# Kernel optimization log

Hardware: AMD Instinct MI355X
Metric: run time of the kernel (lower is better)

## Reference

```python
import jax, jax.numpy as jnp
import numpy as np

V = 32000      # vocab_size
CTX = 1024     # context_length
D = 768        # n_embd
H = 12         # n_heads
HD = D // H    # head_dim
L = 6          # n_layers
DFF = 4 * D
B, S = 2, 1024
EPS = 1e-5


def _layernorm(x, w, b):
    mu = jnp.mean(x, axis=-1, keepdims=True)
    var = jnp.mean(jnp.square(x - mu), axis=-1, keepdims=True)
    return (x - mu) * jax.lax.rsqrt(var + EPS) * w + b


def setup_inputs() -> dict:
    key = jax.random.key(0)
    ks = iter(jax.random.split(key, 32))
    s = 0.02
    idx = jax.random.randint(next(ks), (B, S), 0, V)
    p = {
        "idx": idx,
        "tok_emb": jax.random.normal(next(ks), (V, D), jnp.float32) * s,
        "pos_emb": jax.random.normal(next(ks), (CTX, D), jnp.float32) * s,
        "ln1_w": jnp.ones((L, D)), "ln1_b": jnp.zeros((L, D)),
        "Wq": jax.random.normal(next(ks), (L, D, D), jnp.float32) * s,
        "bq": jnp.zeros((L, D)),
        "Wk": jax.random.normal(next(ks), (L, D, D), jnp.float32) * s,
        "bk": jnp.zeros((L, D)),
        "Wv": jax.random.normal(next(ks), (L, D, D), jnp.float32) * s,
        "bv": jnp.zeros((L, D)),
        "Wo": jax.random.normal(next(ks), (L, D, D), jnp.float32) * s,
        "bo": jnp.zeros((L, D)),
        "ln2_w": jnp.ones((L, D)), "ln2_b": jnp.zeros((L, D)),
        "W1": jax.random.normal(next(ks), (L, D, DFF), jnp.float32) * s,
        "b1": jnp.zeros((L, DFF)),
        "W2": jax.random.normal(next(ks), (L, DFF, D), jnp.float32) * s,
        "b2": jnp.zeros((L, D)),
        "lnf_w": jnp.ones((D,)), "lnf_b": jnp.zeros((D,)),
        "lm_head_w": jax.random.normal(next(ks), (D, V), jnp.float32) * s,
    }
    return p


def _forward(idx, tok_emb, pos_emb, ln1_w, ln1_b, Wq, bq, Wk, bk, Wv, bv,
             Wo, bo, ln2_w, ln2_b, W1, b1, W2, b2, lnf_w, lnf_b, lm_head_w):
    b, s = idx.shape
    x = tok_emb[idx] + pos_emb[:s]  # [B,S,D]
    mask = jnp.tril(jnp.ones((s, s), dtype=bool))  # causal
    scale = 1.0 / np.sqrt(HD)
    for l in range(L):
        # --- attention ---
        h = _layernorm(x, ln1_w[l], ln1_b[l])
        q = (h @ Wq[l] + bq[l]).reshape(b, s, H, HD).transpose(0, 2, 1, 3)
        k = (h @ Wk[l] + bk[l]).reshape(b, s, H, HD).transpose(0, 2, 1, 3)
        v = (h @ Wv[l] + bv[l]).reshape(b, s, H, HD).transpose(0, 2, 1, 3)
        att = jnp.einsum('bhqd,bhkd->bhqk', q, k) * scale
        att = jnp.where(mask, att, -jnp.inf)
        att = jax.nn.softmax(att, axis=-1)
        y = jnp.einsum('bhqk,bhkd->bhqd', att, v)
        y = y.transpose(0, 2, 1, 3).reshape(b, s, D)
        x = x + y @ Wo[l] + bo[l]
        # --- MLP ---
        h2 = _layernorm(x, ln2_w[l], ln2_b[l])
        x = x + jax.nn.relu(h2 @ W1[l] + b1[l]) @ W2[l] + b2[l]
    logits = _layernorm(x, lnf_w, lnf_b) @ lm_head_w  # [B,S,V]
    return logits


def reference(idx, tok_emb, pos_emb, ln1_w, ln1_b, Wq, bq, Wk, bk, Wv, bv,
              Wo, bo, ln2_w, ln2_b, W1, b1, W2, b2, lnf_w, lnf_b, lm_head_w):
    return _forward(idx, tok_emb, pos_emb, ln1_w, ln1_b, Wq, bq, Wk, bk, Wv,
                    bv, Wo, bo, ln2_w, ln2_b, W1, b1, W2, b2, lnf_w, lnf_b,
                    lm_head_w)
```

## Files before the change

### kernel.cpp

```cpp
#include <hip/hip_runtime.h>
#include <hip/hip_bf16.h>
#include <math.h>

#define D 768
#define NH 12
#define HD 64
#define NL 6
#define DFF 3072
#define BB 2
#define SS 1024
#define NROWS (BB*SS)
#define VOCAB 32000
#define QKVN (3*D)
#define LN_EPS 1e-5f

typedef __attribute__((ext_vector_type(8))) short bf16x8;
typedef __attribute__((ext_vector_type(4))) float f32x4;

typedef __attribute__((address_space(1))) const unsigned char* gas_ptr;
typedef __attribute__((address_space(3))) unsigned char* las_ptr;

__device__ __forceinline__ void load_lds16(const void* g, void* l) {
    __builtin_amdgcn_global_load_lds((gas_ptr)g, (las_ptr)l, 16, 0, 0);
}

__device__ __forceinline__ void storeOut(float* p, float v) { *p = v; }
__device__ __forceinline__ void storeOut(__hip_bfloat16* p, float v) { *p = __float2bfloat16(v); }
__device__ __forceinline__ ushort f2bs(float f) {
    __hip_bfloat16 h = __float2bfloat16(f);
    return *(ushort*)&h;
}

__global__ void embed_kernel(const int* __restrict__ idx, const float* __restrict__ tok,
                             const float* __restrict__ pos, float* __restrict__ x) {
    int row = blockIdx.x;
    int s = row % SS;
    int t = idx[row];
    for (int c = threadIdx.x; c < D; c += blockDim.x)
        x[row*D + c] = tok[(size_t)t*D + c] + pos[s*D + c];
}

template<typename OT>
__global__ __launch_bounds__(256) void layernorm_kernel(const float* __restrict__ x,
                                                        const float* __restrict__ w,
                                                        const float* __restrict__ b,
                                                        OT* __restrict__ out) {
    int row = blockIdx.x;
    __shared__ float l1[4], l2[4];
    int base = row * D;
    float vals[3];
    float s1 = 0.f, s2 = 0.f;
#pragma unroll
    for (int i = 0; i < 3; i++) {
        float v = x[base + threadIdx.x + i*256];
        vals[i] = v; s1 += v; s2 += v*v;
    }
#pragma unroll
    for (int o = 32; o > 0; o >>= 1) {
        s1 += __shfl_down(s1, o, 64);
        s2 += __shfl_down(s2, o, 64);
    }
    if ((threadIdx.x & 63) == 0) { l1[threadIdx.x >> 6] = s1; l2[threadIdx.x >> 6] = s2; }
    __syncthreads();
    float sum   = l1[0] + l1[1] + l1[2] + l1[3];
    float sumsq = l2[0] + l2[1] + l2[2] + l2[3];
    float mu  = sum * (1.f / D);
    float var = sumsq * (1.f / D) - mu * mu;
    float inv = rsqrtf(var + LN_EPS);
#pragma unroll
    for (int i = 0; i < 3; i++) {
        int c = threadIdx.x + i*256;
        storeOut(&out[base + c], (vals[i] - mu) * inv * w[c] + b[c]);
    }
}

__global__ __launch_bounds__(256) void transpose_cvt(const float* __restrict__ src,
                                                     __hip_bfloat16* __restrict__ dst,
                                                     int K, int N,
                                                     size_t srcLayerStride, size_t dstLayerStride,
                                                     int dstRowOff) {
    int l = blockIdx.z;
    src += (size_t)l * srcLayerStride;
    dst += (size_t)l * dstLayerStride + (size_t)dstRowOff * K;
    __shared__ float t[32][33];
    int k0 = blockIdx.x*32, n0 = blockIdx.y*32;
    int tx = threadIdx.x & 31, ty = threadIdx.x >> 5;
    for (int i = ty; i < 32; i += 8) t[i][tx] = src[(size_t)(k0+i)*N + n0+tx];
    __syncthreads();
    for (int i = ty; i < 32; i += 8) dst[(size_t)(n0+i)*K + k0+tx] = __float2bfloat16(t[tx][i]);
}

__global__ void pack_qkv_bias(const float* __restrict__ bq, const float* __restrict__ bk,
                              const float* __restrict__ bv, float* __restrict__ dst) {
    int l = blockIdx.y;
    int i = blockIdx.x*256 + threadIdx.x;
    dst[l*QKVN + i]         = bq[l*D + i];
    dst[l*QKVN + D + i]     = bk[l*D + i];
    dst[l*QKVN + 2*D + i]   = bv[l*D + i];
}

template<int BM, int BN, int CMAJ, typename OT, int RELU, int RESID, int HASB>
__global__ __launch_bounds__(256) void gemm_mfma(const ushort* __restrict__ A,
                                                 const ushort* __restrict__ BT,
                                                 const float* __restrict__ bias,
                                                 const float* __restrict__ X,
                                                 OT* __restrict__ C,
                                                 int N, int K, int gx, int gy) {
    constexpr int WTM = BM/2, WTN = BN/2;
    constexpr int FRM = BM/32, FRN = BN/32;
    __shared__ ushort As[BM][32];
    __shared__ ushort Bs[BN][32];

    int id = blockIdx.x;
    int swz = (id & 7) * (gridDim.x >> 3) + (id >> 3);
    int bx, by;
    if (CMAJ) { bx = swz / gy; by = swz - bx * gy; }
    else      { by = swz / gx; bx = swz - by * gx; }
    int bm = by * BM, bn = bx * BN;

    int tid = threadIdx.x;
    int lane = tid & 63, wid = tid >> 6;
    int wr = wid >> 1, wc = wid & 1;
    int lrow = lane >> 2;
    int lcol = (lane & 3) * 8;
    int fr = lane & 15, fc = lane >> 4;

    f32x4 acc[FRM][FRN];
#pragma unroll
    for (int i = 0; i < FRM; i++)
#pragma unroll
        for (int j = 0; j < FRN; j++)
#pragma unroll
            for (int r = 0; r < 4; r++) acc[i][j][r] = 0.f;

    for (int k0 = 0; k0 < K; k0 += 32) {
#pragma unroll
        for (int i = 0; i < BM/64; i++) {
            int rt = wid*(BM/4) + i*16;
            load_lds16(A + (size_t)(bm + rt + lrow)*K + k0 + lcol, &As[rt][0]);
        }
#pragma unroll
        for (int i = 0; i < BN/64; i++) {
            int rt = wid*(BN/4) + i*16;
            load_lds16(BT + (size_t)(bn + rt + lrow)*K + k0 + lcol, &Bs[rt][0]);
        }
        asm volatile("s_waitcnt vmcnt(0)" ::: "memory");
        __syncthreads();
        bf16x8 af[FRM], bf[FRN];
#pragma unroll
        for (int mi = 0; mi < FRM; mi++) af[mi] = *(const bf16x8*)&As[wr*WTM + mi*16 + fr][fc*8];
#pragma unroll
        for (int ni = 0; ni < FRN; ni++) bf[ni] = *(const bf16x8*)&Bs[wc*WTN + ni*16 + fr][fc*8];
#pragma unroll
        for (int mi = 0; mi < FRM; mi++)
#pragma unroll
            for (int ni = 0; ni < FRN; ni++)
                acc[mi][ni] = __builtin_amdgcn_mfma_f32_16x16x32_bf16(af[mi], bf[ni], acc[mi][ni], 0, 0, 0);
        __syncthreads();
    }
#pragma unroll
    for (int mi = 0; mi < FRM; mi++) {
#pragma unroll
        for (int r = 0; r < 4; r++) {
            int row = bm + wr*WTM + mi*16 + fc*4 + r;
#pragma unroll
            for (int ni = 0; ni < FRN; ni++) {
                int col = bn + wc*WTN + ni*16 + fr;
                float v = acc[mi][ni][r];
                if (HASB) v += bias[col];
                if (RESID) v += X[(size_t)row * N + col];
                if (RELU) v = fmaxf(v, 0.f);
                storeOut(&C[(size_t)row * N + col], v);
            }
        }
    }
}

__global__ __launch_bounds__(256) void attn_mfma(const float* __restrict__ qkv,
                                                 __hip_bfloat16* __restrict__ y) {
    const int bx = blockIdx.x;
    const int qt = 15 - (bx & 15);
    const int h  = (bx >> 4) % NH;
    const int b  = bx / (16*NH);
    const int tid  = threadIdx.x;
    const int lane = tid & 63, w = tid >> 6;
    const int fr = lane & 15, fc = lane >> 4;

    __shared__ ushort Qs[64][72];
    __shared__ ushort Ks[64][72];
    __shared__ ushort Vs[64][72];
    __shared__ ushort Ps[4][16][72];

    const int q0 = qt * 64;
    const int srow = tid >> 2, sfs = tid & 3;

    {
        const float* src = qkv + (size_t)(b*SS + q0 + srow)*QKVN + h*HD;
#pragma unroll
        for (int it = 0; it < 4; it++) {
            int d0 = sfs*4 + it*16;
            float4 v4 = *(const float4*)(src + d0);
            ushort4 u;
            u.x = f2bs(v4.x); u.y = f2bs(v4.y); u.z = f2bs(v4.z); u.w = f2bs(v4.w);
            *(ushort4*)&Qs[srow][d0] = u;
        }
    }
    bf16x8 qf[2];
#pragma unroll
    for (int s = 0; s < 2; s++) qf[s] = *(const bf16x8*)&Qs[w*16 + fr][s*32 + fc*8];

    f32x4 oacc[4];
#pragma unroll
    for (int ni = 0; ni < 4; ni++)
#pragma unroll
        for (int r = 0; r < 4; r++) oacc[ni][r] = 0.f;
    float m[4] = {-INFINITY, -INFINITY, -INFINITY, -INFINITY};
    float l[4] = {0.f, 0.f, 0.f, 0.f};

    for (int kt = 0; kt <= qt; kt++) {
        const int kv0 = kt * 64;
        __syncthreads();
        {
            const float* ksrc = qkv + (size_t)(b*SS + kv0 + srow)*QKVN + D   + h*HD;
            const float* vsrc = qkv + (size_t)(b*SS + kv0 + srow)*QKVN + 2*D + h*HD;
#pragma unroll
            for (int it = 0; it < 4; it++) {
                int d0 = sfs*4 + it*16;
                float4 kv4 = *(const float4*)(ksrc + d0);
                ushort4 u;
                u.x = f2bs(kv4.x); u.y = f2bs(kv4.y); u.z = f2bs(kv4.z); u.w = f2bs(kv4.w);
                *(ushort4*)&Ks[srow][d0] = u;
                float4 vv4 = *(const float4*)(vsrc + d0);
                Vs[d0+0][srow] = f2bs(vv4.x);
                Vs[d0+1][srow] = f2bs(vv4.y);
                Vs[d0+2][srow] = f2bs(vv4.z);
                Vs[d0+3][srow] = f2bs(vv4.w);
            }
        }
        __syncthreads();
        f32x4 sacc[4];
#pragma unroll
        for (int ni = 0; ni < 4; ni++)
#pragma unroll
            for (int r = 0; r < 4; r++) sacc[ni][r] = 0.f;
#pragma unroll
        for (int ni = 0; ni < 4; ni++)
#pragma unroll
            for (int s = 0; s < 2; s++) {
                bf16x8 kf = *(const bf16x8*)&Ks[ni*16 + fr][s*32 + fc*8];
                sacc[ni] = __builtin_amdgcn_mfma_f32_16x16x32_bf16(qf[s], kf, sacc[ni], 0, 0, 0);
            }
        if (kt == qt) {
#pragma unroll
            for (int ni = 0; ni < 4; ni++)
#pragma unroll
                for (int r = 0; r < 4; r++) {
                    float v = sacc[ni][r] * 0.125f;
                    sacc[ni][r] = (ni*16 + fr > w*16 + fc*4 + r) ? -INFINITY : v;
                }
        } else {
#pragma unroll
            for (int ni = 0; ni < 4; ni++)
#pragma unroll
                for (int r = 0; r < 4; r++) sacc[ni][r] *= 0.125f;
        }
        float p[4][4];
#pragma unroll
        for (int r = 0; r < 4; r++) {
            float mx = fmaxf(fmaxf(sacc[0][r], sacc[1][r]), fmaxf(sacc[2][r], sacc[3][r]));
#pragma unroll
            for (int o = 1; o < 16; o <<= 1) mx = fmaxf(mx, __shfl_xor(mx, o, 64));
            float mn = fmaxf(m[r], mx);
            float fac = __expf(m[r] - mn);
            float rs = 0.f;
#pragma unroll
            for (int ni = 0; ni < 4; ni++) {
                float pv = __expf(sacc[ni][r] - mn);
                p[ni][r] = pv;
                rs += pv;
            }
#pragma unroll
            for (int o = 1; o < 16; o <<= 1) rs += __shfl_xor(rs, o, 64);
            l[r] = l[r] * fac + rs;
            m[r] = mn;
#pragma unroll
            for (int ni = 0; ni < 4; ni++) oacc[ni][r] *= fac;
        }
#pragma unroll
        for (int ni = 0; ni < 4; ni++)
#pragma unroll
            for (int r = 0; r < 4; r++)
                Ps[w][fc*4 + r][ni*16 + fr] = f2bs(p[ni][r]);
        bf16x8 pa[2];
#pragma unroll
        for (int s = 0; s < 2; s++) pa[s] = *(const bf16x8*)&Ps[w][fr][s*32 + fc*8];
#pragma unroll
        for (int ni = 0; ni < 4; ni++)
#pragma unroll
            for (int s = 0; s < 2; s++) {
                bf16x8 vf = *(const bf16x8*)&Vs[ni*16 + fr][s*32 + fc*8];
                oacc[ni] = __builtin_amdgcn_mfma_f32_16x16x32_bf16(pa[s], vf, oacc[ni], 0, 0, 0);
            }
    }
#pragma unroll
    for (int r = 0; r < 4; r++) {
        float rinv = 1.f / l[r];
        int row = b*SS + q0 + w*16 + fc*4 + r;
#pragma unroll
        for (int ni = 0; ni < 4; ni++)
            y[(size_t)row*D + h*HD + ni*16 + fr] = __float2bfloat16(oacc[ni][r] * rinv);
    }
}

extern "C" void kernel_launch(void* const* d_in, const int* in_sizes, int n_in,
                              void* d_out, int out_size, void* d_ws, size_t ws_size,
                              hipStream_t stream) {
    const int*   idx  = (const int*)d_in[0];
    const float* tok  = (const float*)d_in[1];
    const float* pos  = (const float*)d_in[2];
    const float* ln1w = (const float*)d_in[3];
    const float* ln1b = (const float*)d_in[4];
    const float* Wq   = (const float*)d_in[5];
    const float* bq   = (const float*)d_in[6];
    const float* Wk   = (const float*)d_in[7];
    const float* bk   = (const float*)d_in[8];
    const float* Wv   = (const float*)d_in[9];
    const float* bv   = (const float*)d_in[10];
    const float* Wo   = (const float*)d_in[11];
    const float* bo   = (const float*)d_in[12];
    const float* ln2w = (const float*)d_in[13];
    const float* ln2b = (const float*)d_in[14];
    const float* W1   = (const float*)d_in[15];
    const float* b1   = (const float*)d_in[16];
    const float* W2   = (const float*)d_in[17];
    const float* b2   = (const float*)d_in[18];
    const float* lnfw = (const float*)d_in[19];
    const float* lnfb = (const float*)d_in[20];
    const float* lmw  = (const float*)d_in[21];
    float* out = (float*)d_out;

    char* p = (char*)d_ws;
    __hip_bfloat16* qkvT = (__hip_bfloat16*)p; p += (size_t)NL*QKVN*D*2;
    __hip_bfloat16* WoT  = (__hip_bfloat16*)p; p += (size_t)NL*D*D*2;
    __hip_bfloat16* W1T  = (__hip_bfloat16*)p; p += (size_t)NL*DFF*D*2;
    __hip_bfloat16* W2T  = (__hip_bfloat16*)p; p += (size_t)NL*D*DFF*2;
    __hip_bfloat16* lmT  = (__hip_bfloat16*)p; p += (size_t)VOCAB*D*2;
    float*          bqkv = (float*)p;          p += (size_t)NL*QKVN*4;
    float*          x    = (float*)p;          p += (size_t)NROWS*D*4;
    __hip_bfloat16* h    = (__hip_bfloat16*)p; p += (size_t)NROWS*D*2;
    float*          qkv  = (float*)p;          p += (size_t)NROWS*QKVN*4;
    __hip_bfloat16* yb   = (__hip_bfloat16*)p; p += (size_t)NROWS*D*2;
    __hip_bfloat16* a1   = (__hip_bfloat16*)p; p += (size_t)NROWS*DFF*2;

    dim3 tDD(D/32, D/32, NL);
    transpose_cvt<<<tDD, 256, 0, stream>>>(Wq, qkvT, D, D, (size_t)D*D, (size_t)QKVN*D, 0);
    transpose_cvt<<<tDD, 256, 0, stream>>>(Wk, qkvT, D, D, (size_t)D*D, (size_t)QKVN*D, D);
    transpose_cvt<<<tDD, 256, 0, stream>>>(Wv, qkvT, D, D, (size_t)D*D, (size_t)QKVN*D, 2*D);
    transpose_cvt<<<tDD, 256, 0, stream>>>(Wo, WoT, D, D, (size_t)D*D, (size_t)D*D, 0);
    transpose_cvt<<<dim3(D/32, DFF/32, NL), 256, 0, stream>>>(W1, W1T, D, DFF, (size_t)D*DFF, (size_t)DFF*D, 0);
    transpose_cvt<<<dim3(DFF/32, D/32, NL), 256, 0, stream>>>(W2, W2T, DFF, D, (size_t)DFF*D, (size_t)D*DFF, 0);
    transpose_cvt<<<dim3(D/32, VOCAB/32, 1), 256, 0, stream>>>(lmw, lmT, D, VOCAB, 0, 0, 0);
    pack_qkv_bias<<<dim3(3, NL), 256, 0, stream>>>(bq, bk, bv, bqkv);

    embed_kernel<<<NROWS, 256, 0, stream>>>(idx, tok, pos, x);

    for (int l = 0; l < NL; l++) {
        layernorm_kernel<<<NROWS, 256, 0, stream>>>(x, ln1w + l*D, ln1b + l*D, h);
        gemm_mfma<128,64,0,float,0,0,1><<<576, 256, 0, stream>>>(
            (const ushort*)h, (const ushort*)(qkvT + (size_t)l*QKVN*D),
            bqkv + (size_t)l*QKVN, nullptr, qkv, QKVN, D, QKVN/64, NROWS/128);
        attn_mfma<<<BB*NH*(SS/64), 256, 0, stream>>>(qkv, yb);
        gemm_mfma<64,64,0,float,0,1,1><<<384, 256, 0, stream>>>(
            (const ushort*)yb, (const ushort*)(WoT + (size_t)l*D*D),
            bo + (size_t)l*D, x, x, D, D, D/64, NROWS/64);
        layernorm_kernel<<<NROWS, 256, 0, stream>>>(x, ln2w + l*D, ln2b + l*D, h);
        gemm_mfma<128,128,0,__hip_bfloat16,1,0,1><<<384, 256, 0, stream>>>(
            (const ushort*)h, (const ushort*)(W1T + (size_t)l*DFF*D),
            b1 + (size_t)l*DFF, nullptr, a1, DFF, D, DFF/128, NROWS/128);
        gemm_mfma<64,64,0,float,0,1,1><<<384, 256, 0, stream>>>(
            (const ushort*)a1, (const ushort*)(W2T + (size_t)l*D*DFF),
            b2 + (size_t)l*D, x, x, D, DFF, D/64, NROWS/64);
    }
    layernorm_kernel<<<NROWS, 256, 0, stream>>>(x, lnfw, lnfb, h);
    gemm_mfma<128,128,1,float,0,0,0><<<4000, 256, 0, stream>>>(
        (const ushort*)h, (const ushort*)lmT, nullptr, nullptr, out, VOCAB, D,
        VOCAB/128, NROWS/128);
}
```

Baseline: 1.408 ms.

## Store QKV in bf16, pre-transpose V, and XOR-swizzle LDS tiles

The QKV projection now writes bf16 instead of fp32, which halves that buffer's traffic. A new kernel transposes V into a per-head [HD][S] layout so attention can fill its K/V/Q tiles with direct global-to-LDS loads instead of scalar convert-and-scatter code. LDS tiles in both the GEMM and the attention kernel use an XOR chunk swizzle to avoid bank conflicts, and the attention tiles drop their padding. The cost is an extra kernel launch per layer and more bf16 rounding on Q/K/V.

New measurement: 1.277 ms. -9.3%, faster.

```diff
diff --git a/kernel.cpp b/kernel.cpp
--- a/kernel.cpp
+++ b/kernel.cpp
@@ -90,6 +90,22 @@
     for (int i = ty; i < 32; i += 8) dst[(size_t)(n0+i)*K + k0+tx] = __float2bfloat16(t[tx][i]);
 }
 
+__global__ __launch_bounds__(256) void vtrans_kernel(const ushort* __restrict__ qkv,
+                                                     ushort* __restrict__ vt) {
+    int bh = blockIdx.z;
+    int st = blockIdx.y;
+    int dt = blockIdx.x;
+    __shared__ ushort t[32][33];
+    int tx = threadIdx.x & 31, ty = threadIdx.x >> 5;
+    int b = bh / NH, h = bh % NH;
+    int s0 = st*32, d0 = dt*32;
+    for (int i = ty; i < 32; i += 8)
+        t[i][tx] = qkv[(size_t)(b*SS + s0+i)*QKVN + 2*D + h*HD + d0 + tx];
+    __syncthreads();
+    for (int i = ty; i < 32; i += 8)
+        vt[((size_t)bh*HD + d0+i)*SS + s0 + tx] = t[tx][i];
+}
+
 __global__ void pack_qkv_bias(const float* __restrict__ bq, const float* __restrict__ bk,
                               const float* __restrict__ bv, float* __restrict__ dst) {
     int l = blockIdx.y;
@@ -122,7 +138,7 @@
     int lane = tid & 63, wid = tid >> 6;
     int wr = wid >> 1, wc = wid & 1;
     int lrow = lane >> 2;
-    int lcol = (lane & 3) * 8;
+    int lcol = (((lane & 3) ^ (lrow & 3)) * 8);
     int fr = lane & 15, fc = lane >> 4;
 
     f32x4 acc[FRM][FRN];
@@ -148,9 +164,11 @@
         __syncthreads();
         bf16x8 af[FRM], bf[FRN];
 #pragma unroll
-        for (int mi = 0; mi < FRM; mi++) af[mi] = *(const bf16x8*)&As[wr*WTM + mi*16 + fr][fc*8];
-#pragma unroll
-        for (int ni = 0; ni < FRN; ni++) bf[ni] = *(const bf16x8*)&Bs[wc*WTN + ni*16 + fr][fc*8];
+        for (int mi = 0; mi < FRM; mi++)
+            af[mi] = *(const bf16x8*)&As[wr*WTM + mi*16 + fr][(fc ^ (fr & 3))*8];
+#pragma unroll
+        for (int ni = 0; ni < FRN; ni++)
+            bf[ni] = *(const bf16x8*)&Bs[wc*WTN + ni*16 + fr][(fc ^ (fr & 3))*8];
 #pragma unroll
         for (int mi = 0; mi < FRM; mi++)
 #pragma unroll
@@ -176,7 +194,8 @@
     }
 }
 
-__global__ __launch_bounds__(256) void attn_mfma(const float* __restrict__ qkv,
+__global__ __launch_bounds__(256) void attn_mfma(const ushort* __restrict__ qkv,
+                                                 const ushort* __restrict__ vt,
                                                  __hip_bfloat16* __restrict__ y) {
     const int bx = blockIdx.x;
     const int qt = 15 - (bx & 15);
@@ -186,28 +205,25 @@
     const int lane = tid & 63, w = tid >> 6;
     const int fr = lane & 15, fc = lane >> 4;
 
-    __shared__ ushort Qs[64][72];
-    __shared__ ushort Ks[64][72];
-    __shared__ ushort Vs[64][72];
+    __shared__ ushort Qs[64][64];
+    __shared__ ushort Ks[64][64];
+    __shared__ ushort Vs[64][64];
     __shared__ ushort Ps[4][16][72];
 
     const int q0 = qt * 64;
-    const int srow = tid >> 2, sfs = tid & 3;
-
-    {
-        const float* src = qkv + (size_t)(b*SS + q0 + srow)*QKVN + h*HD;
-#pragma unroll
-        for (int it = 0; it < 4; it++) {
-            int d0 = sfs*4 + it*16;
-            float4 v4 = *(const float4*)(src + d0);
-            ushort4 u;
-            u.x = f2bs(v4.x); u.y = f2bs(v4.y); u.z = f2bs(v4.z); u.w = f2bs(v4.w);
-            *(ushort4*)&Qs[srow][d0] = u;
-        }
-    }
+    const int srow8  = lane >> 3;
+    const int schunk = (lane & 7) ^ srow8;
+
+#pragma unroll
+    for (int j = 0; j < 2; j++) {
+        int r = w*16 + j*8 + srow8;
+        load_lds16(qkv + (size_t)(b*SS + q0 + r)*QKVN + h*HD + schunk*8, &Qs[w*16 + j*8][0]);
+    }
+    asm volatile("s_waitcnt vmcnt(0)" ::: "memory");
     bf16x8 qf[2];
 #pragma unroll
-    for (int s = 0; s < 2; s++) qf[s] = *(const bf16x8*)&Qs[w*16 + fr][s*32 + fc*8];
+    for (int s = 0; s < 2; s++)
+        qf[s] = *(const bf16x8*)&Qs[w*16 + fr][((s*4 + fc) ^ (fr & 7))*8];
 
     f32x4 oacc[4];
 #pragma unroll
@@ -220,23 +236,13 @@
     for (int kt = 0; kt <= qt; kt++) {
         const int kv0 = kt * 64;
         __syncthreads();
-        {
-            const float* ksrc = qkv + (size_t)(b*SS + kv0 + srow)*QKVN + D   + h*HD;
-            const float* vsrc = qkv + (size_t)(b*SS + kv0 + srow)*QKVN + 2*D + h*HD;
-#pragma unroll
-            for (int it = 0; it < 4; it++) {
-                int d0 = sfs*4 + it*16;
-                float4 kv4 = *(const float4*)(ksrc + d0);
-                ushort4 u;
-                u.x = f2bs(kv4.x); u.y = f2bs(kv4.y); u.z = f2bs(kv4.z); u.w = f2bs(kv4.w);
-                *(ushort4*)&Ks[srow][d0] = u;
-                float4 vv4 = *(const float4*)(vsrc + d0);
-                Vs[d0+0][srow] = f2bs(vv4.x);
-                Vs[d0+1][srow] = f2bs(vv4.y);
-                Vs[d0+2][srow] = f2bs(vv4.z);
-                Vs[d0+3][srow] = f2bs(vv4.w);
-            }
-        }
+#pragma unroll
+        for (int j = 0; j < 2; j++) {
+            int r = w*16 + j*8 + srow8;
+            load_lds16(qkv + (size_t)(b*SS + kv0 + r)*QKVN + D + h*HD + schunk*8, &Ks[w*16 + j*8][0]);
+            load_lds16(vt + ((size_t)(b*NH + h)*HD + r)*SS + kv0 + schunk*8, &Vs[w*16 + j*8][0]);
+        }
+        asm volatile("s_waitcnt vmcnt(0)" ::: "memory");
         __syncthreads();
         f32x4 sacc[4];
 #pragma unroll
@@ -247,7 +253,7 @@
         for (int ni = 0; ni < 4; ni++)
 #pragma unroll
             for (int s = 0; s < 2; s++) {
-                bf16x8 kf = *(const bf16x8*)&Ks[ni*16 + fr][s*32 + fc*8];
+                bf16x8 kf = *(const bf16x8*)&Ks[ni*16 + fr][((s*4 + fc) ^ (fr & 7))*8];
                 sacc[ni] = __builtin_amdgcn_mfma_f32_16x16x32_bf16(qf[s], kf, sacc[ni], 0, 0, 0);
             }
         if (kt == qt) {
@@ -298,7 +304,7 @@
         for (int ni = 0; ni < 4; ni++)
 #pragma unroll
             for (int s = 0; s < 2; s++) {
-                bf16x8 vf = *(const bf16x8*)&Vs[ni*16 + fr][s*32 + fc*8];
+                bf16x8 vf = *(const bf16x8*)&Vs[ni*16 + fr][((s*4 + fc) ^ (fr & 7))*8];
                 oacc[ni] = __builtin_amdgcn_mfma_f32_16x16x32_bf16(pa[s], vf, oacc[ni], 0, 0, 0);
             }
     }
@@ -348,7 +354,8 @@
     float*          bqkv = (float*)p;          p += (size_t)NL*QKVN*4;
     float*          x    = (float*)p;          p += (size_t)NROWS*D*4;
     __hip_bfloat16* h    = (__hip_bfloat16*)p; p += (size_t)NROWS*D*2;
-    float*          qkv  = (float*)p;          p += (size_t)NROWS*QKVN*4;
+    __hip_bfloat16* qkv  = (__hip_bfloat16*)p; p += (size_t)NROWS*QKVN*2;
+    __hip_bfloat16* vt   = (__hip_bfloat16*)p; p += (size_t)BB*NH*HD*SS*2;
     __hip_bfloat16* yb   = (__hip_bfloat16*)p; p += (size_t)NROWS*D*2;
     __hip_bfloat16* a1   = (__hip_bfloat16*)p; p += (size_t)NROWS*DFF*2;
 
@@ -366,10 +373,11 @@
 
     for (int l = 0; l < NL; l++) {
         layernorm_kernel<<<NROWS, 256, 0, stream>>>(x, ln1w + l*D, ln1b + l*D, h);
-        gemm_mfma<128,64,0,float,0,0,1><<<576, 256, 0, stream>>>(
+        gemm_mfma<128,64,0,__hip_bfloat16,0,0,1><<<576, 256, 0, stream>>>(
             (const ushort*)h, (const ushort*)(qkvT + (size_t)l*QKVN*D),
             bqkv + (size_t)l*QKVN, nullptr, qkv, QKVN, D, QKVN/64, NROWS/128);
-        attn_mfma<<<BB*NH*(SS/64), 256, 0, stream>>>(qkv, yb);
+        vtrans_kernel<<<dim3(2, SS/32, BB*NH), 256, 0, stream>>>((const ushort*)qkv, (ushort*)vt);
+        attn_mfma<<<BB*NH*(SS/64), 256, 0, stream>>>((const ushort*)qkv, (const ushort*)vt, yb);
         gemm_mfma<64,64,0,float,0,1,1><<<384, 256, 0, stream>>>(
             (const ushort*)yb, (const ushort*)(WoT + (size_t)l*D*D),
             bo + (size_t)l*D, x, x, D, D, D/64, NROWS/64);
```
